# Kernel tuning notes

Measured on AMD Instinct MI355X. Metric: run time of the kernel, lower is better.

Reference implementation:

```python
import jax, jax.numpy as jnp
import numpy as np

B, L, E, H, D = 32, 512, 256, 8, 64
SCALE = int(D ** 0.5)  # matches TF: int(hidden_dim ** 0.5) == 8


def setup_inputs() -> dict:
    key = jax.random.key(0)
    ks = jax.random.split(key, 6)
    return {
        "x": jax.random.normal(ks[0], (B, L, E), dtype=jnp.float32),
        "positional": jax.random.normal(ks[1], (L, E), dtype=jnp.float32) * 0.02,
        "Wq": jax.random.normal(ks[2], (H, E, D), dtype=jnp.float32) * 0.05,
        "Wk": jax.random.normal(ks[3], (H, E, D), dtype=jnp.float32) * 0.05,
        "Wv": jax.random.normal(ks[4], (H, E, D), dtype=jnp.float32) * 0.05,
        "Wo": jax.random.normal(ks[5], (H * D, E), dtype=jnp.float32) * 0.05,
    }


def reference(x, positional, Wq, Wk, Wv, Wo):
    act = jnp.tanh  # activation='tanh'
    xp = x + positional                                   # [B,L,E]
    # Batched per-head projections with activation applied post-matmul
    q = act(jnp.einsum('ble,hed->bhld', xp, Wq))          # [B,H,L,D]
    k = act(jnp.einsum('ble,hed->bhld', xp, Wk))
    v = act(jnp.einsum('ble,hed->bhld', xp, Wv))
    score = jnp.einsum('bhqd,bhkd->bhqk', q, k) / SCALE   # [B,H,L,L]
    attn = jax.nn.softmax(score, axis=-1)
    out = jnp.einsum('bhqk,bhkd->bhqd', attn, v)          # [B,H,L,D]
    # concat heads along last axis (head-major) -> [B,L,H*D]
    out = jnp.transpose(out, (0, 2, 1, 3)).reshape(B, L, H * D)
    return jnp.einsum('blf,fe->ble', out, Wo) + act(xp)   # [B,L,E]
```

## Files before the change

### kernel.cpp

```cpp
#include <hip/hip_runtime.h>
#include <cstdint>

#define NB 32
#define NL 512
#define NE 256
#define NH 8
#define ND 64
#define NM 16384
#define NHD 512

using half8  = __attribute__((ext_vector_type(8))) _Float16;
using half4  = __attribute__((ext_vector_type(4))) _Float16;
using f32x4  = __attribute__((ext_vector_type(4))) float;
using f32x16 = __attribute__((ext_vector_type(16))) float;
using u32x2  = __attribute__((ext_vector_type(2))) unsigned int;

__device__ __forceinline__ f32x4 mfma16(half8 a, half8 b, f32x4 c) {
    return __builtin_amdgcn_mfma_f32_16x16x32_f16(a, b, c, 0, 0, 0);
}
__device__ __forceinline__ f32x16 mfma32(half8 a, half8 b, f32x16 c) {
    return __builtin_amdgcn_mfma_f32_32x32x16_f16(a, b, c, 0, 0, 0);
}
__device__ __forceinline__ void cp16_g2l(const void* g, void* l) {
    __builtin_amdgcn_global_load_lds(
        (const __attribute__((address_space(1))) void*)g,
        (__attribute__((address_space(3))) void*)l, 16, 0, 0);
}
__device__ __forceinline__ float exp2fast(float x) {
    return __builtin_amdgcn_exp2f(x);
}
__device__ __forceinline__ float fast_tanh(float x) {
    float xc = fminf(fmaxf(x, -9.f), 9.f);
    float t = exp2fast(xc * 2.88539008178f);
    return (t - 1.f) * __builtin_amdgcn_rcpf(t + 1.f);
}
__device__ __forceinline__ uint32_t pk16(float a, float b) {
    auto h2 = __builtin_amdgcn_cvt_pkrtz(a, b);
    return __builtin_bit_cast(uint32_t, h2);
}

__global__ __launch_bounds__(256) void prep(
        const float* __restrict__ x, const float* __restrict__ pos,
        const float* __restrict__ Wq, const float* __restrict__ Wk,
        const float* __restrict__ Wv, const float* __restrict__ Wo,
        _Float16* __restrict__ wqkv, _Float16* __restrict__ woh,
        _Float16* __restrict__ xph) {
    int bid = blockIdx.x;
    if (bid < 2048) {
        int idx = bid * 256 + threadIdx.x;
        if (idx < 1536 * 256) {
            int n = idx >> 8, e = idx & 255;
            int s = n >> 9, h = (n >> 6) & 7, d = n & 63;
            const float* W = (s == 0) ? Wq : (s == 1) ? Wk : Wv;
            wqkv[idx] = (_Float16)W[(h * NE + e) * ND + d];
        } else {
            int j = idx - 1536 * 256;
            int e = j >> 9, f = j & 511;
            woh[j] = (_Float16)Wo[f * NE + e];
        }
    } else {
        int i = ((bid - 2048) * 256 + threadIdx.x) * 4;
        float4 xv = *(const float4*)(x + i);
        float4 pv = *(const float4*)(pos + (i & (NL * NE - 1)));
        half4 o;
        o[0] = (_Float16)(xv.x + pv.x);
        o[1] = (_Float16)(xv.y + pv.y);
        o[2] = (_Float16)(xv.z + pv.z);
        o[3] = (_Float16)(xv.w + pv.w);
        *(half4*)(xph + i) = o;
    }
}

__global__ __launch_bounds__(1024)
__attribute__((amdgpu_waves_per_eu(4, 4))) void attn_fused(
        const _Float16* __restrict__ wqkv, const _Float16* __restrict__ xph,
        _Float16* __restrict__ attn_out) {
    __shared__ _Float16 Kp[512 * 64];
    __shared__ _Float16 Vtp[64 * 512];
    __shared__ _Float16 Wst[2 * 64 * 64];
    _Float16* Xs = Vtp;

    int tid = threadIdx.x;
    int w = tid >> 6, l = tid & 63;
    int l31 = l & 31, hi = l >> 5;
    int g0 = ((blockIdx.x & 7) << 5) + (blockIdx.x >> 3);
    int h = g0 & 7, b = g0 >> 3;
    const float C1 = 0.125f * 1.44269504089f;
    const float C4 = 4.f * 1.44269504089f;

    int lrow8 = l >> 3;
    int kc16 = (l & 7) ^ lrow8;
    const _Float16* xg = xph + (size_t)(b * NL) * 256;
    const _Float16* wgq = wqkv + (size_t)(h * 64) * 256;
    const _Float16* wgk = wgq + (size_t)512 * 256;
    const _Float16* wgv = wgq + (size_t)1024 * 256;

    f32x16 acc_q[2] = {}, acc_k[2] = {};
    for (int kt2 = 0; kt2 < 4; ++kt2) {
#pragma unroll
        for (int j = 0; j < 4; ++j) {
            int c = j * 16 + w;
            cp16_g2l(xg + (size_t)(c * 8 + lrow8) * 256 + kt2 * 64 + kc16 * 8,
                     Xs + c * 512);
        }
        {
            const _Float16* ws = (w < 8) ? wgq : wgk;
            int row = (w & 7) * 8 + lrow8;
            cp16_g2l(ws + (size_t)row * 256 + kt2 * 64 + kc16 * 8, Wst + w * 512);
        }
        __syncthreads();
        int rowb = w * 32 + l31;
#pragma unroll
        for (int ks2 = 0; ks2 < 4; ++ks2) {
            int u = ks2 * 2 + hi;
            half8 bf = *(const half8*)(Xs + rowb * 64 + ((u ^ (rowb & 7)) << 3));
#pragma unroll
            for (int d2 = 0; d2 < 2; ++d2) {
                int ra = d2 * 32 + l31;
                int sa = ra * 64 + ((u ^ (ra & 7)) << 3);
                half8 aq = *(const half8*)(Wst + sa);
                half8 ak = *(const half8*)(Wst + 4096 + sa);
                acc_q[d2] = mfma32(aq, bf, acc_q[d2]);
                acc_k[d2] = mfma32(ak, bf, acc_k[d2]);
            }
        }
        __syncthreads();
    }
    half8 qf[4];
    {
        int row = w * 32 + l31;
#pragma unroll
        for (int ks = 0; ks < 4; ++ks) {
            int d2 = ks >> 1, s = ks & 1;
            uint32_t qe0 = pk16(fast_tanh(acc_q[d2][8 * s + 0]), fast_tanh(acc_q[d2][8 * s + 1]));
            uint32_t qe1 = pk16(fast_tanh(acc_q[d2][8 * s + 2]), fast_tanh(acc_q[d2][8 * s + 3]));
            uint32_t qo0 = pk16(fast_tanh(acc_q[d2][8 * s + 4]), fast_tanh(acc_q[d2][8 * s + 5]));
            uint32_t qo1 = pk16(fast_tanh(acc_q[d2][8 * s + 6]), fast_tanh(acc_q[d2][8 * s + 7]));
            uint32_t ke0 = pk16(fast_tanh(acc_k[d2][8 * s + 0]), fast_tanh(acc_k[d2][8 * s + 1]));
            uint32_t ke1 = pk16(fast_tanh(acc_k[d2][8 * s + 2]), fast_tanh(acc_k[d2][8 * s + 3]));
            uint32_t ko0 = pk16(fast_tanh(acc_k[d2][8 * s + 4]), fast_tanh(acc_k[d2][8 * s + 5]));
            uint32_t ko1 = pk16(fast_tanh(acc_k[d2][8 * s + 6]), fast_tanh(acc_k[d2][8 * s + 7]));
            u32x2 q0 = __builtin_amdgcn_permlane32_swap(qe0, qo0, false, false);
            u32x2 q1 = __builtin_amdgcn_permlane32_swap(qe1, qo1, false, false);
            u32x2 k0 = __builtin_amdgcn_permlane32_swap(ke0, ko0, false, false);
            u32x2 k1 = __builtin_amdgcn_permlane32_swap(ke1, ko1, false, false);
            union { uint32_t u[4]; half8 h8; } pq, pk;
            pq.u[0] = q0[0]; pq.u[1] = q1[0]; pq.u[2] = q0[1]; pq.u[3] = q1[1];
            pk.u[0] = k0[0]; pk.u[1] = k1[0]; pk.u[2] = k0[1]; pk.u[3] = k1[1];
            qf[ks] = pq.h8;
            int uu = ks * 2 + hi;
            *(half8*)(Kp + row * 64 + ((uu ^ (row & 7)) << 3)) = pk.h8;
        }
    }
    __syncthreads();

    f32x16 acc_v[2] = {};
    int kb = w >> 1, d2w = w & 1;
    for (int kt2 = 0; kt2 < 4; ++kt2) {
#pragma unroll
        for (int j = 0; j < 4; ++j) {
            int c = j * 16 + w;
            cp16_g2l(xg + (size_t)(c * 8 + lrow8) * 256 + kt2 * 64 + kc16 * 8,
                     Xs + c * 512);
        }
        if (w < 8) {
            int row = w * 8 + lrow8;
            cp16_g2l(wgv + (size_t)row * 256 + kt2 * 64 + kc16 * 8, Wst + w * 512);
        }
        __syncthreads();
#pragma unroll
        for (int ks2 = 0; ks2 < 4; ++ks2) {
            int u = ks2 * 2 + hi;
            int rw = d2w * 32 + l31;
            half8 wv = *(const half8*)(Wst + rw * 64 + ((u ^ (rw & 7)) << 3));
#pragma unroll
            for (int kb2 = 0; kb2 < 2; ++kb2) {
                int rx = kb * 64 + kb2 * 32 + l31;
                half8 xa = *(const half8*)(Xs + rx * 64 + ((u ^ (rx & 7)) << 3));
                acc_v[kb2] = mfma32(xa, wv, acc_v[kb2]);
            }
        }
        __syncthreads();
    }
    {
        int d = d2w * 32 + l31;
#pragma unroll
        for (int ks = 0; ks < 4; ++ks) {
            int kb2 = ks >> 1, s = ks & 1;
            uint32_t ve0 = pk16(fast_tanh(acc_v[kb2][8 * s + 0]), fast_tanh(acc_v[kb2][8 * s + 1]));
            uint32_t ve1 = pk16(fast_tanh(acc_v[kb2][8 * s + 2]), fast_tanh(acc_v[kb2][8 * s + 3]));
            uint32_t vo0 = pk16(fast_tanh(acc_v[kb2][8 * s + 4]), fast_tanh(acc_v[kb2][8 * s + 5]));
            uint32_t vo1 = pk16(fast_tanh(acc_v[kb2][8 * s + 6]), fast_tanh(acc_v[kb2][8 * s + 7]));
            u32x2 v0 = __builtin_amdgcn_permlane32_swap(ve0, vo0, false, false);
            u32x2 v1 = __builtin_amdgcn_permlane32_swap(ve1, vo1, false, false);
            union { uint32_t u[4]; half8 h8; } pv;
            pv.u[0] = v0[0]; pv.u[1] = v1[0]; pv.u[2] = v0[1]; pv.u[3] = v1[1];
            int guu = kb * 8 + kb2 * 4 + s * 2 + hi;
            *(half8*)(Vtp + d * 512 + ((guu ^ (d & 7)) << 3)) = pv.h8;
        }
    }
    __syncthreads();

    f32x16 acc_o[2] = {};
    float lrow = 0.f;
    for (int kt = 0; kt < 8; ++kt) {
        f32x16 acc_s[2] = {};
        __builtin_amdgcn_s_setprio(1);
#pragma unroll
        for (int ks = 0; ks < 4; ++ks)
#pragma unroll
            for (int kb2 = 0; kb2 < 2; ++kb2) {
                int key = kt * 64 + kb2 * 32 + l31;
                half8 kbf = *(const half8*)(Kp + key * 64 + (((ks * 2 + hi) ^ (key & 7)) << 3));
                acc_s[kb2] = mfma32(kbf, qf[ks], acc_s[kb2]);
            }
        __builtin_amdgcn_s_setprio(0);
        float rs = 0.f;
#pragma unroll
        for (int ks = 0; ks < 4; ++ks) {
            int kb2 = ks >> 1, s = ks & 1;
            float p0 = exp2fast(fmaf(acc_s[kb2][8 * s + 0], C1, -C4));
            float p1 = exp2fast(fmaf(acc_s[kb2][8 * s + 1], C1, -C4));
            float p2 = exp2fast(fmaf(acc_s[kb2][8 * s + 2], C1, -C4));
            float p3 = exp2fast(fmaf(acc_s[kb2][8 * s + 3], C1, -C4));
            float p4 = exp2fast(fmaf(acc_s[kb2][8 * s + 4], C1, -C4));
            float p5 = exp2fast(fmaf(acc_s[kb2][8 * s + 5], C1, -C4));
            float p6 = exp2fast(fmaf(acc_s[kb2][8 * s + 6], C1, -C4));
            float p7 = exp2fast(fmaf(acc_s[kb2][8 * s + 7], C1, -C4));
            rs += ((p0 + p1) + (p2 + p3)) + ((p4 + p5) + (p6 + p7));
            uint32_t we0 = pk16(p0, p1), we1 = pk16(p2, p3);
            uint32_t wo0 = pk16(p4, p5), wo1 = pk16(p6, p7);
            u32x2 r0 = __builtin_amdgcn_permlane32_swap(we0, wo0, false, false);
            u32x2 r1 = __builtin_amdgcn_permlane32_swap(we1, wo1, false, false);
            union { uint32_t u[4]; half8 h8; } pu;
            pu.u[0] = r0[0]; pu.u[1] = r1[0]; pu.u[2] = r0[1]; pu.u[3] = r1[1];
            __builtin_amdgcn_s_setprio(1);
#pragma unroll
            for (int d2 = 0; d2 < 2; ++d2) {
                int d = d2 * 32 + l31;
                int uu = kt * 8 + ks * 2 + hi;
                half8 vb = *(const half8*)(Vtp + d * 512 + ((uu ^ (d & 7)) << 3));
                acc_o[d2] = mfma32(pu.h8, vb, acc_o[d2]);
            }
            __builtin_amdgcn_s_setprio(0);
        }
        lrow += rs;
    }
    lrow += __shfl_xor(lrow, 32);
    size_t orow0 = (size_t)(b * NL + w * 32);
#pragma unroll
    for (int c = 0; c < 4; ++c)
#pragma unroll
        for (int r = 0; r < 4; ++r) {
            int qrow = c * 8 + hi * 4 + r;
            float inv = 1.f / __shfl(lrow, qrow);
#pragma unroll
            for (int d2 = 0; d2 < 2; ++d2)
                attn_out[(orow0 + qrow) * NHD + h * ND + d2 * 32 + l31] =
                    (_Float16)(acc_o[d2][c * 4 + r] * inv);
        }
}

__global__ __launch_bounds__(256) void final_gemm(
        const _Float16* __restrict__ woh, const _Float16* __restrict__ attn,
        const _Float16* __restrict__ xph, float* __restrict__ out) {
    __shared__ _Float16 Alds[2][128 * 64];
    __shared__ _Float16 Blds[2][64 * 64];
    int tid = threadIdx.x;
    int w = tid >> 6, l = tid & 63;
    int bid = blockIdx.x;
    int xcd = bid & 7, local = bid >> 3;
    int tn = local & 1;
    int tm = xcd * 32 + (local >> 1);
    int wn = w >> 1, wm = w & 1;
    int m16 = l & 15, g = l >> 4;
    int lrow8 = l >> 3;
    int kc16 = (l & 7) ^ lrow8;
    f32x4 acc[4][2] = {};

    const _Float16* Ag = woh + (size_t)tn * 128 * 512;
    const _Float16* Bg = attn + (size_t)tm * 64 * 512;

#define FIN_STAGE(kt, buf)                                                    \
    _Pragma("unroll") for (int i = 0; i < 4; ++i) {                           \
        int cA = w * 4 + i;                                                   \
        int row = cA * 8 + lrow8;                                             \
        cp16_g2l(Ag + (size_t)row * 512 + (kt) * 64 + kc16 * 8,               \
                 &Alds[buf][cA * 512]);                                       \
    }                                                                         \
    _Pragma("unroll") for (int i = 0; i < 2; ++i) {                           \
        int cB = w * 2 + i;                                                   \
        int row = cB * 8 + lrow8;                                             \
        cp16_g2l(Bg + (size_t)row * 512 + (kt) * 64 + kc16 * 8,               \
                 &Blds[buf][cB * 512]);                                       \
    }

    FIN_STAGE(0, 0);
    __syncthreads();
    int cur = 0;
    for (int kt = 0; kt < 8; ++kt) {
        if (kt < 7) { FIN_STAGE(kt + 1, cur ^ 1); }
#pragma unroll
        for (int ks = 0; ks < 2; ++ks) {
            half8 af[4], bf[2];
#pragma unroll
            for (int f = 0; f < 4; ++f) {
                int ra = wn * 64 + f * 16 + m16;
                af[f] = *(const half8*)(&Alds[cur][ra * 64 + (((ks * 4 + g) ^ (ra & 7)) << 3)]);
            }
#pragma unroll
            for (int f = 0; f < 2; ++f) {
                int rb = wm * 32 + f * 16 + m16;
                bf[f] = *(const half8*)(&Blds[cur][rb * 64 + (((ks * 4 + g) ^ (rb & 7)) << 3)]);
            }
#pragma unroll
            for (int nf = 0; nf < 4; ++nf)
#pragma unroll
                for (int mf = 0; mf < 2; ++mf)
                    acc[nf][mf] = mfma16(af[nf], bf[mf], acc[nf][mf]);
        }
        __syncthreads();
        cur ^= 1;
    }
#undef FIN_STAGE
#pragma unroll
    for (int nf = 0; nf < 4; ++nf) {
        int e = tn * 128 + wn * 64 + nf * 16 + g * 4;
#pragma unroll
        for (int mf = 0; mf < 2; ++mf) {
            int m = tm * 64 + wm * 32 + mf * 16 + m16;
            half4 hx = *(const half4*)(xph + (size_t)m * NE + e);
            f32x4 v = acc[nf][mf];
            float4 o;
            o.x = v[0] + fast_tanh((float)hx[0]);
            o.y = v[1] + fast_tanh((float)hx[1]);
            o.z = v[2] + fast_tanh((float)hx[2]);
            o.w = v[3] + fast_tanh((float)hx[3]);
            *(float4*)(out + (size_t)m * NE + e) = o;
        }
    }
}

extern "C" void kernel_launch(void* const* d_in, const int* in_sizes, int n_in,
                              void* d_out, int out_size, void* d_ws, size_t ws_size,
                              hipStream_t stream) {
    const float* x   = (const float*)d_in[0];
    const float* pos = (const float*)d_in[1];
    const float* Wq  = (const float*)d_in[2];
    const float* Wk  = (const float*)d_in[3];
    const float* Wv  = (const float*)d_in[4];
    const float* Wo  = (const float*)d_in[5];
    float* out = (float*)d_out;

    char* ws = (char*)d_ws;
    _Float16* xph   = (_Float16*)(ws);
    _Float16* wqkv  = (_Float16*)(ws + 8388608);
    _Float16* woh   = (_Float16*)(ws + 9175040);
    _Float16* attn  = (_Float16*)(ws + 9437184);

    prep<<<dim3(6144), dim3(256), 0, stream>>>(x, pos, Wq, Wk, Wv, Wo, wqkv, woh, xph);
    attn_fused<<<dim3(256), dim3(1024), 0, stream>>>(wqkv, xph, attn);
    final_gemm<<<dim3(512), dim3(256), 0, stream>>>(woh, attn, xph, out);
}
```

Baseline: 75.29 us.

## Split attention per query half with two-phase key/value recompute

Each attention block now covers one query half (256 rows) of one (batch, head) pair, which doubles the grid to 512 blocks of 512 threads. Keys and values are processed in two 256-row phases that share one staged buffer, and LDS per block is halved. The intent is better CU occupancy and load balance, allowing two blocks per CU. In exchange, the K and V projections are computed twice per (batch, head), once by each query-half block, which adds MFMA work and extra global reads of x.

```diff
diff --git a/kernel.cpp b/kernel.cpp
--- a/kernel.cpp
+++ b/kernel.cpp
@@ -71,183 +71,198 @@
     }
 }
 
-__global__ __launch_bounds__(1024)
-__attribute__((amdgpu_waves_per_eu(4, 4))) void attn_fused(
+__global__ __launch_bounds__(512, 2) void attn_fused(
         const _Float16* __restrict__ wqkv, const _Float16* __restrict__ xph,
         _Float16* __restrict__ attn_out) {
-    __shared__ _Float16 Kp[512 * 64];
-    __shared__ _Float16 Vtp[64 * 512];
+    __shared__ _Float16 Kp[256 * 64];
+    __shared__ _Float16 XV[256 * 64];
     __shared__ _Float16 Wst[2 * 64 * 64];
-    _Float16* Xs = Vtp;
+    _Float16* Xs  = XV;
+    _Float16* Vtp = XV;
 
     int tid = threadIdx.x;
     int w = tid >> 6, l = tid & 63;
     int l31 = l & 31, hi = l >> 5;
-    int g0 = ((blockIdx.x & 7) << 5) + (blockIdx.x >> 3);
-    int h = g0 & 7, b = g0 >> 3;
+    int g0 = ((blockIdx.x & 7) << 6) + (blockIdx.x >> 3);
+    int b = g0 >> 4, h = (g0 >> 1) & 7, qh = g0 & 1;
     const float C1 = 0.125f * 1.44269504089f;
     const float C4 = 4.f * 1.44269504089f;
 
     int lrow8 = l >> 3;
     int kc16 = (l & 7) ^ lrow8;
-    const _Float16* xg = xph + (size_t)(b * NL) * 256;
     const _Float16* wgq = wqkv + (size_t)(h * 64) * 256;
     const _Float16* wgk = wgq + (size_t)512 * 256;
     const _Float16* wgv = wgq + (size_t)1024 * 256;
 
-    f32x16 acc_q[2] = {}, acc_k[2] = {};
-    for (int kt2 = 0; kt2 < 4; ++kt2) {
-#pragma unroll
-        for (int j = 0; j < 4; ++j) {
-            int c = j * 16 + w;
-            cp16_g2l(xg + (size_t)(c * 8 + lrow8) * 256 + kt2 * 64 + kc16 * 8,
-                     Xs + c * 512);
-        }
-        {
-            const _Float16* ws = (w < 8) ? wgq : wgk;
-            int row = (w & 7) * 8 + lrow8;
-            cp16_g2l(ws + (size_t)row * 256 + kt2 * 64 + kc16 * 8, Wst + w * 512);
-        }
-        __syncthreads();
-        int rowb = w * 32 + l31;
-#pragma unroll
-        for (int ks2 = 0; ks2 < 4; ++ks2) {
-            int u = ks2 * 2 + hi;
-            half8 bf = *(const half8*)(Xs + rowb * 64 + ((u ^ (rowb & 7)) << 3));
-#pragma unroll
-            for (int d2 = 0; d2 < 2; ++d2) {
-                int ra = d2 * 32 + l31;
-                int sa = ra * 64 + ((u ^ (ra & 7)) << 3);
-                half8 aq = *(const half8*)(Wst + sa);
-                half8 ak = *(const half8*)(Wst + 4096 + sa);
-                acc_q[d2] = mfma32(aq, bf, acc_q[d2]);
-                acc_k[d2] = mfma32(ak, bf, acc_k[d2]);
-            }
-        }
-        __syncthreads();
-    }
+    int kb = w >> 1, d2w = w & 1;
     half8 qf[4];
-    {
-        int row = w * 32 + l31;
-#pragma unroll
-        for (int ks = 0; ks < 4; ++ks) {
-            int d2 = ks >> 1, s = ks & 1;
-            uint32_t qe0 = pk16(fast_tanh(acc_q[d2][8 * s + 0]), fast_tanh(acc_q[d2][8 * s + 1]));
-            uint32_t qe1 = pk16(fast_tanh(acc_q[d2][8 * s + 2]), fast_tanh(acc_q[d2][8 * s + 3]));
-            uint32_t qo0 = pk16(fast_tanh(acc_q[d2][8 * s + 4]), fast_tanh(acc_q[d2][8 * s + 5]));
-            uint32_t qo1 = pk16(fast_tanh(acc_q[d2][8 * s + 6]), fast_tanh(acc_q[d2][8 * s + 7]));
-            uint32_t ke0 = pk16(fast_tanh(acc_k[d2][8 * s + 0]), fast_tanh(acc_k[d2][8 * s + 1]));
-            uint32_t ke1 = pk16(fast_tanh(acc_k[d2][8 * s + 2]), fast_tanh(acc_k[d2][8 * s + 3]));
-            uint32_t ko0 = pk16(fast_tanh(acc_k[d2][8 * s + 4]), fast_tanh(acc_k[d2][8 * s + 5]));
-            uint32_t ko1 = pk16(fast_tanh(acc_k[d2][8 * s + 6]), fast_tanh(acc_k[d2][8 * s + 7]));
-            u32x2 q0 = __builtin_amdgcn_permlane32_swap(qe0, qo0, false, false);
-            u32x2 q1 = __builtin_amdgcn_permlane32_swap(qe1, qo1, false, false);
-            u32x2 k0 = __builtin_amdgcn_permlane32_swap(ke0, ko0, false, false);
-            u32x2 k1 = __builtin_amdgcn_permlane32_swap(ke1, ko1, false, false);
-            union { uint32_t u[4]; half8 h8; } pq, pk;
-            pq.u[0] = q0[0]; pq.u[1] = q1[0]; pq.u[2] = q0[1]; pq.u[3] = q1[1];
-            pk.u[0] = k0[0]; pk.u[1] = k1[0]; pk.u[2] = k0[1]; pk.u[3] = k1[1];
-            qf[ks] = pq.h8;
-            int uu = ks * 2 + hi;
-            *(half8*)(Kp + row * 64 + ((uu ^ (row & 7)) << 3)) = pk.h8;
-        }
-    }
-    __syncthreads();
-
-    f32x16 acc_v[2] = {};
-    int kb = w >> 1, d2w = w & 1;
-    for (int kt2 = 0; kt2 < 4; ++kt2) {
-#pragma unroll
-        for (int j = 0; j < 4; ++j) {
-            int c = j * 16 + w;
-            cp16_g2l(xg + (size_t)(c * 8 + lrow8) * 256 + kt2 * 64 + kc16 * 8,
-                     Xs + c * 512);
-        }
-        if (w < 8) {
-            int row = w * 8 + lrow8;
-            cp16_g2l(wgv + (size_t)row * 256 + kt2 * 64 + kc16 * 8, Wst + w * 512);
-        }
-        __syncthreads();
-#pragma unroll
-        for (int ks2 = 0; ks2 < 4; ++ks2) {
-            int u = ks2 * 2 + hi;
-            int rw = d2w * 32 + l31;
-            half8 wv = *(const half8*)(Wst + rw * 64 + ((u ^ (rw & 7)) << 3));
-#pragma unroll
-            for (int kb2 = 0; kb2 < 2; ++kb2) {
-                int rx = kb * 64 + kb2 * 32 + l31;
-                half8 xa = *(const half8*)(Xs + rx * 64 + ((u ^ (rx & 7)) << 3));
-                acc_v[kb2] = mfma32(xa, wv, acc_v[kb2]);
-            }
-        }
-        __syncthreads();
-    }
-    {
-        int d = d2w * 32 + l31;
-#pragma unroll
-        for (int ks = 0; ks < 4; ++ks) {
-            int kb2 = ks >> 1, s = ks & 1;
-            uint32_t ve0 = pk16(fast_tanh(acc_v[kb2][8 * s + 0]), fast_tanh(acc_v[kb2][8 * s + 1]));
-            uint32_t ve1 = pk16(fast_tanh(acc_v[kb2][8 * s + 2]), fast_tanh(acc_v[kb2][8 * s + 3]));
-            uint32_t vo0 = pk16(fast_tanh(acc_v[kb2][8 * s + 4]), fast_tanh(acc_v[kb2][8 * s + 5]));
-            uint32_t vo1 = pk16(fast_tanh(acc_v[kb2][8 * s + 6]), fast_tanh(acc_v[kb2][8 * s + 7]));
-            u32x2 v0 = __builtin_amdgcn_permlane32_swap(ve0, vo0, false, false);
-            u32x2 v1 = __builtin_amdgcn_permlane32_swap(ve1, vo1, false, false);
-            union { uint32_t u[4]; half8 h8; } pv;
-            pv.u[0] = v0[0]; pv.u[1] = v1[0]; pv.u[2] = v0[1]; pv.u[3] = v1[1];
-            int guu = kb * 8 + kb2 * 4 + s * 2 + hi;
-            *(half8*)(Vtp + d * 512 + ((guu ^ (d & 7)) << 3)) = pv.h8;
-        }
-    }
-    __syncthreads();
-
     f32x16 acc_o[2] = {};
     float lrow = 0.f;
-    for (int kt = 0; kt < 8; ++kt) {
-        f32x16 acc_s[2] = {};
-        __builtin_amdgcn_s_setprio(1);
-#pragma unroll
-        for (int ks = 0; ks < 4; ++ks)
-#pragma unroll
-            for (int kb2 = 0; kb2 < 2; ++kb2) {
-                int key = kt * 64 + kb2 * 32 + l31;
-                half8 kbf = *(const half8*)(Kp + key * 64 + (((ks * 2 + hi) ^ (key & 7)) << 3));
-                acc_s[kb2] = mfma32(kbf, qf[ks], acc_s[kb2]);
-            }
-        __builtin_amdgcn_s_setprio(0);
-        float rs = 0.f;
-#pragma unroll
-        for (int ks = 0; ks < 4; ++ks) {
-            int kb2 = ks >> 1, s = ks & 1;
-            float p0 = exp2fast(fmaf(acc_s[kb2][8 * s + 0], C1, -C4));
-            float p1 = exp2fast(fmaf(acc_s[kb2][8 * s + 1], C1, -C4));
-            float p2 = exp2fast(fmaf(acc_s[kb2][8 * s + 2], C1, -C4));
-            float p3 = exp2fast(fmaf(acc_s[kb2][8 * s + 3], C1, -C4));
-            float p4 = exp2fast(fmaf(acc_s[kb2][8 * s + 4], C1, -C4));
-            float p5 = exp2fast(fmaf(acc_s[kb2][8 * s + 5], C1, -C4));
-            float p6 = exp2fast(fmaf(acc_s[kb2][8 * s + 6], C1, -C4));
-            float p7 = exp2fast(fmaf(acc_s[kb2][8 * s + 7], C1, -C4));
-            rs += ((p0 + p1) + (p2 + p3)) + ((p4 + p5) + (p6 + p7));
-            uint32_t we0 = pk16(p0, p1), we1 = pk16(p2, p3);
-            uint32_t wo0 = pk16(p4, p5), wo1 = pk16(p6, p7);
-            u32x2 r0 = __builtin_amdgcn_permlane32_swap(we0, wo0, false, false);
-            u32x2 r1 = __builtin_amdgcn_permlane32_swap(we1, wo1, false, false);
-            union { uint32_t u[4]; half8 h8; } pu;
-            pu.u[0] = r0[0]; pu.u[1] = r1[0]; pu.u[2] = r0[1]; pu.u[3] = r1[1];
+
+#pragma unroll
+    for (int ph = 0; ph < 2; ++ph) {
+        int kh = qh ^ ph;
+        const _Float16* xg = xph + (size_t)(b * NL + kh * 256) * 256;
+
+        f32x16 acc_a[2] = {}, acc_k[2] = {};
+        for (int kt2 = 0; kt2 < 4; ++kt2) {
+#pragma unroll
+            for (int j = 0; j < 4; ++j) {
+                int c = w * 4 + j;
+                cp16_g2l(xg + (size_t)(c * 8 + lrow8) * 256 + kt2 * 64 + kc16 * 8,
+                         Xs + c * 512);
+            }
+            {
+                int row = w * 8 + lrow8;
+                cp16_g2l(wgk + (size_t)row * 256 + kt2 * 64 + kc16 * 8,
+                         Wst + w * 512);
+                if (ph == 0)
+                    cp16_g2l(wgq + (size_t)row * 256 + kt2 * 64 + kc16 * 8,
+                             Wst + 4096 + w * 512);
+            }
+            __syncthreads();
+            int rowb = w * 32 + l31;
+#pragma unroll
+            for (int ks2 = 0; ks2 < 4; ++ks2) {
+                int u = ks2 * 2 + hi;
+                half8 bf = *(const half8*)(Xs + rowb * 64 + ((u ^ (rowb & 7)) << 3));
+#pragma unroll
+                for (int d2 = 0; d2 < 2; ++d2) {
+                    int ra = d2 * 32 + l31;
+                    int sa = ra * 64 + ((u ^ (ra & 7)) << 3);
+                    half8 ak = *(const half8*)(Wst + sa);
+                    acc_k[d2] = mfma32(ak, bf, acc_k[d2]);
+                    if (ph == 0) {
+                        half8 aq = *(const half8*)(Wst + 4096 + sa);
+                        acc_a[d2] = mfma32(aq, bf, acc_a[d2]);
+                    }
+                }
+            }
+            __syncthreads();
+        }
+        {
+            int row = w * 32 + l31;
+#pragma unroll
+            for (int ks = 0; ks < 4; ++ks) {
+                int d2 = ks >> 1, s = ks & 1;
+                uint32_t ke0 = pk16(fast_tanh(acc_k[d2][8 * s + 0]), fast_tanh(acc_k[d2][8 * s + 1]));
+                uint32_t ke1 = pk16(fast_tanh(acc_k[d2][8 * s + 2]), fast_tanh(acc_k[d2][8 * s + 3]));
+                uint32_t ko0 = pk16(fast_tanh(acc_k[d2][8 * s + 4]), fast_tanh(acc_k[d2][8 * s + 5]));
+                uint32_t ko1 = pk16(fast_tanh(acc_k[d2][8 * s + 6]), fast_tanh(acc_k[d2][8 * s + 7]));
+                u32x2 k0 = __builtin_amdgcn_permlane32_swap(ke0, ko0, false, false);
+                u32x2 k1 = __builtin_amdgcn_permlane32_swap(ke1, ko1, false, false);
+                union { uint32_t u[4]; half8 h8; } pk;
+                pk.u[0] = k0[0]; pk.u[1] = k1[0]; pk.u[2] = k0[1]; pk.u[3] = k1[1];
+                int uu = ks * 2 + hi;
+                *(half8*)(Kp + row * 64 + ((uu ^ (row & 7)) << 3)) = pk.h8;
+                if (ph == 0) {
+                    uint32_t qe0 = pk16(fast_tanh(acc_a[d2][8 * s + 0]), fast_tanh(acc_a[d2][8 * s + 1]));
+                    uint32_t qe1 = pk16(fast_tanh(acc_a[d2][8 * s + 2]), fast_tanh(acc_a[d2][8 * s + 3]));
+                    uint32_t qo0 = pk16(fast_tanh(acc_a[d2][8 * s + 4]), fast_tanh(acc_a[d2][8 * s + 5]));
+                    uint32_t qo1 = pk16(fast_tanh(acc_a[d2][8 * s + 6]), fast_tanh(acc_a[d2][8 * s + 7]));
+                    u32x2 q0 = __builtin_amdgcn_permlane32_swap(qe0, qo0, false, false);
+                    u32x2 q1 = __builtin_amdgcn_permlane32_swap(qe1, qo1, false, false);
+                    union { uint32_t u[4]; half8 h8; } pq;
+                    pq.u[0] = q0[0]; pq.u[1] = q1[0]; pq.u[2] = q0[1]; pq.u[3] = q1[1];
+                    qf[ks] = pq.h8;
+                }
+            }
+        }
+        f32x16 acc_v[2] = {};
+        for (int kt2 = 0; kt2 < 4; ++kt2) {
+#pragma unroll
+            for (int j = 0; j < 4; ++j) {
+                int c = w * 4 + j;
+                cp16_g2l(xg + (size_t)(c * 8 + lrow8) * 256 + kt2 * 64 + kc16 * 8,
+                         Xs + c * 512);
+            }
+            {
+                int row = w * 8 + lrow8;
+                cp16_g2l(wgv + (size_t)row * 256 + kt2 * 64 + kc16 * 8,
+                         Wst + w * 512);
+            }
+            __syncthreads();
+#pragma unroll
+            for (int ks2 = 0; ks2 < 4; ++ks2) {
+                int u = ks2 * 2 + hi;
+                int rw = d2w * 32 + l31;
+                half8 wv = *(const half8*)(Wst + rw * 64 + ((u ^ (rw & 7)) << 3));
+#pragma unroll
+                for (int kb2 = 0; kb2 < 2; ++kb2) {
+                    int rx = kb * 64 + kb2 * 32 + l31;
+                    half8 xa = *(const half8*)(Xs + rx * 64 + ((u ^ (rx & 7)) << 3));
+                    acc_v[kb2] = mfma32(xa, wv, acc_v[kb2]);
+                }
+            }
+            __syncthreads();
+        }
+        {
+            int d = d2w * 32 + l31;
+#pragma unroll
+            for (int ks = 0; ks < 4; ++ks) {
+                int kb2 = ks >> 1, s = ks & 1;
+                uint32_t ve0 = pk16(fast_tanh(acc_v[kb2][8 * s + 0]), fast_tanh(acc_v[kb2][8 * s + 1]));
+                uint32_t ve1 = pk16(fast_tanh(acc_v[kb2][8 * s + 2]), fast_tanh(acc_v[kb2][8 * s + 3]));
+                uint32_t vo0 = pk16(fast_tanh(acc_v[kb2][8 * s + 4]), fast_tanh(acc_v[kb2][8 * s + 5]));
+                uint32_t vo1 = pk16(fast_tanh(acc_v[kb2][8 * s + 6]), fast_tanh(acc_v[kb2][8 * s + 7]));
+                u32x2 v0 = __builtin_amdgcn_permlane32_swap(ve0, vo0, false, false);
+                u32x2 v1 = __builtin_amdgcn_permlane32_swap(ve1, vo1, false, false);
+                union { uint32_t u[4]; half8 h8; } pv;
+                pv.u[0] = v0[0]; pv.u[1] = v1[0]; pv.u[2] = v0[1]; pv.u[3] = v1[1];
+                int guu = kb * 8 + kb2 * 4 + s * 2 + hi;
+                *(half8*)(Vtp + d * 256 + ((guu ^ (d & 7)) << 3)) = pv.h8;
+            }
+        }
+        __syncthreads();
+
+        for (int kt = 0; kt < 4; ++kt) {
+            f32x16 acc_s[2] = {};
             __builtin_amdgcn_s_setprio(1);
 #pragma unroll
-            for (int d2 = 0; d2 < 2; ++d2) {
-                int d = d2 * 32 + l31;
-                int uu = kt * 8 + ks * 2 + hi;
-                half8 vb = *(const half8*)(Vtp + d * 512 + ((uu ^ (d & 7)) << 3));
-                acc_o[d2] = mfma32(pu.h8, vb, acc_o[d2]);
-            }
+            for (int ks = 0; ks < 4; ++ks)
+#pragma unroll
+                for (int kb2 = 0; kb2 < 2; ++kb2) {
+                    int key = kt * 64 + kb2 * 32 + l31;
+                    half8 kbf = *(const half8*)(Kp + key * 64 + (((ks * 2 + hi) ^ (key & 7)) << 3));
+                    acc_s[kb2] = mfma32(kbf, qf[ks], acc_s[kb2]);
+                }
             __builtin_amdgcn_s_setprio(0);
-        }
-        lrow += rs;
-    }
+            float rs = 0.f;
+#pragma unroll
+            for (int ks = 0; ks < 4; ++ks) {
+                int kb2 = ks >> 1, s = ks & 1;
+                float p0 = exp2fast(fmaf(acc_s[kb2][8 * s + 0], C1, -C4));
+                float p1 = exp2fast(fmaf(acc_s[kb2][8 * s + 1], C1, -C4));
+                float p2 = exp2fast(fmaf(acc_s[kb2][8 * s + 2], C1, -C4));
+                float p3 = exp2fast(fmaf(acc_s[kb2][8 * s + 3], C1, -C4));
+                float p4 = exp2fast(fmaf(acc_s[kb2][8 * s + 4], C1, -C4));
+                float p5 = exp2fast(fmaf(acc_s[kb2][8 * s + 5], C1, -C4));
+                float p6 = exp2fast(fmaf(acc_s[kb2][8 * s + 6], C1, -C4));
+                float p7 = exp2fast(fmaf(acc_s[kb2][8 * s + 7], C1, -C4));
+                rs += ((p0 + p1) + (p2 + p3)) + ((p4 + p5) + (p6 + p7));
+                uint32_t we0 = pk16(p0, p1), we1 = pk16(p2, p3);
+                uint32_t wo0 = pk16(p4, p5), wo1 = pk16(p6, p7);
+                u32x2 r0 = __builtin_amdgcn_permlane32_swap(we0, wo0, false, false);
+                u32x2 r1 = __builtin_amdgcn_permlane32_swap(we1, wo1, false, false);
+                union { uint32_t u[4]; half8 h8; } pu;
+                pu.u[0] = r0[0]; pu.u[1] = r1[0]; pu.u[2] = r0[1]; pu.u[3] = r1[1];
+                __builtin_amdgcn_s_setprio(1);
+#pragma unroll
+                for (int d2 = 0; d2 < 2; ++d2) {
+                    int d = d2 * 32 + l31;
+                    int uu = kt * 8 + ks * 2 + hi;
+                    half8 vb = *(const half8*)(Vtp + d * 256 + ((uu ^ (d & 7)) << 3));
+                    acc_o[d2] = mfma32(pu.h8, vb, acc_o[d2]);
+                }
+                __builtin_amdgcn_s_setprio(0);
+            }
+            lrow += rs;
+        }
+        __syncthreads();
+    }
+
     lrow += __shfl_xor(lrow, 32);
-    size_t orow0 = (size_t)(b * NL + w * 32);
+    size_t orow0 = (size_t)(b * NL + qh * 256 + w * 32);
 #pragma unroll
     for (int c = 0; c < 4; ++c)
 #pragma unroll
@@ -359,6 +374,6 @@
     _Float16* attn  = (_Float16*)(ws + 9437184);
 
     prep<<<dim3(6144), dim3(256), 0, stream>>>(x, pos, Wq, Wk, Wv, Wo, wqkv, woh, xph);
-    attn_fused<<<dim3(256), dim3(1024), 0, stream>>>(wqkv, xph, attn);
+    attn_fused<<<dim3(512), dim3(512), 0, stream>>>(wqkv, xph, attn);
     final_gemm<<<dim3(512), dim3(256), 0, stream>>>(woh, attn, xph, out);
 }
```

Measured after the change: 114.5 us. +52.1%, slower.
